# Kernel tuning notes

Hardware: AMD Instinct MI355X
Metric: run time of the kernel (lower is better)

Reference implementation:

```python
import jax, jax.numpy as jnp
import numpy as np

N_NODES = 50000
N_EDGES = 800000
N_GRAPHS = 512
IN_DIM, HID_DIM, EMB_DIM = 128, 256, 128
EPS = 1e-5


def setup_inputs() -> dict:
    key = jax.random.key(0)
    ks = jax.random.split(key, 12)
    x = jax.random.normal(ks[0], (N_NODES, IN_DIM), dtype=jnp.float32)
    edge_index = jax.random.randint(ks[1], (2, N_EDGES), 0, N_NODES, dtype=jnp.int32)
    batch = jnp.sort(jax.random.randint(ks[2], (N_NODES,), 0, N_GRAPHS, dtype=jnp.int32))
    s1 = 1.0 / np.sqrt(IN_DIM)
    s2 = 1.0 / np.sqrt(HID_DIM)
    return {
        "x": x,
        "edge_index": edge_index,
        "batch": batch,
        "W1": jax.random.uniform(ks[3], (IN_DIM, HID_DIM), jnp.float32, -s1, s1),
        "b1": jnp.zeros((HID_DIM,), jnp.float32),
        "gamma1": jnp.ones((HID_DIM,), jnp.float32),
        "beta1": jnp.zeros((HID_DIM,), jnp.float32),
        "W2": jax.random.uniform(ks[4], (HID_DIM, EMB_DIM), jnp.float32, -s2, s2),
        "b2": jnp.zeros((EMB_DIM,), jnp.float32),
        "gamma2": jnp.ones((EMB_DIM,), jnp.float32),
        "beta2": jnp.zeros((EMB_DIM,), jnp.float32),
    }


def _gcn_conv(x, W, b, src, dst, n_nodes):
    # PyG GCNConv: h = xW; aggregate with sym-normalized adjacency incl. self-loops; + bias
    h = x @ W  # [N, D]
    ones = jnp.ones(src.shape[0], dtype=h.dtype)
    deg = jax.ops.segment_sum(ones, dst, num_segments=n_nodes) + 1.0  # self-loop
    dinv = jax.lax.rsqrt(deg)
    norm = dinv[src] * dinv[dst]  # [E]
    msg = h[src] * norm[:, None]  # gather + scale  [E, D]
    agg = jax.ops.segment_sum(msg, dst, num_segments=n_nodes)
    agg = agg + h * (1.0 / deg)[:, None]  # self-loop contribution (norm = 1/deg)
    return agg + b


def _batchnorm(h, gamma, beta):
    mean = jnp.mean(h, axis=0)
    var = jnp.mean(jnp.square(h - mean), axis=0)  # biased, training mode
    return gamma * (h - mean) * jax.lax.rsqrt(var + EPS) + beta


def reference(x, edge_index, batch, W1, b1, gamma1, beta1, W2, b2, gamma2, beta2):
    src, dst = edge_index[0], edge_index[1]
    n = x.shape[0]
    h = _gcn_conv(x, W1, b1, src, dst, n)
    h = _batchnorm(jax.nn.relu(h), gamma1, beta1)
    h = _gcn_conv(h, W2, b2, src, dst, n)
    h = _batchnorm(jax.nn.relu(h), gamma2, beta2)
    return jax.ops.segment_max(h, batch, num_segments=N_GRAPHS)
```

## Files before the change

### kernel.cpp

```cpp
#include <hip/hip_runtime.h>
#include <math.h>

#define N_NODES 50000
#define N_EDGES 800000
#define N_GRAPHS 512
#define IN_DIM 128
#define HID_DIM 256
#define EMB_DIM 128
#define EPS 1e-5f
#define ELLW 64
#define NGROUP 8
#define GROUPN 6250
#define BLK_PER_GROUP 256
#define EPB ((N_EDGES + BLK_PER_GROUP - 1) / BLK_PER_GROUP)
#define F2B_N (N_NODES * IN_DIM / 4)
#define F2B_BLOCKS ((F2B_N + 255) / 256)
#define TW1_BLOCKS ((HID_DIM * IN_DIM + 255) / 256)

typedef __attribute__((ext_vector_type(8))) short bf16x8;
typedef __attribute__((ext_vector_type(4))) float f32x4;

static __device__ __forceinline__ unsigned short f2b(float f) {
    unsigned u = __float_as_uint(f);
    return (unsigned short)((u + 0x7fffu + ((u >> 16) & 1u)) >> 16);
}
static __device__ __forceinline__ float b2f(unsigned short h) {
    return __uint_as_float(((unsigned)h) << 16);
}

__global__ void __launch_bounds__(256) scatter_xcd(const int* __restrict__ src,
                                                   const int* __restrict__ dst,
                                                   int* __restrict__ fill,
                                                   int* __restrict__ col) {
    int b = blockIdx.x;
    int g = b & 7;
    int bs = b >> 3;
    int lo = g * GROUPN;
    int hi = lo + GROUPN;
    int e_end = min((bs + 1) * EPB, N_EDGES);
    for (int e = bs * EPB + threadIdx.x; e < e_end; e += 256) {
        int d = dst[e];
        if (d >= lo && d < hi) {
            int pos = atomicAdd(&fill[d], 1);
            pos = min(pos, ELLW - 1);
            col[(d << 6) + pos] = src[e];
        }
    }
}

__global__ void dinv_kernel(const int* __restrict__ fill, float* __restrict__ dinv) {
    int v = blockIdx.x * blockDim.x + threadIdx.x;
    if (v < N_NODES) dinv[v] = rsqrtf((float)(min(fill[v], ELLW) + 1));
}

__global__ void convert_kernel(const float* __restrict__ x, unsigned short* __restrict__ xbf,
                               const float* __restrict__ W1, unsigned short* __restrict__ W1t) {
    int b = blockIdx.x;
    if (b < F2B_BLOCKS) {
        int i = b * 256 + threadIdx.x;
        if (i < F2B_N) {
            float4 v = ((const float4*)x)[i];
            ushort4 o;
            o.x = f2b(v.x); o.y = f2b(v.y); o.z = f2b(v.z); o.w = f2b(v.w);
            ((ushort4*)xbf)[i] = o;
        }
    } else {
        int j = (b - F2B_BLOCKS) * 256 + threadIdx.x;
        if (j < HID_DIM * IN_DIM) {
            int n = j >> 7;
            int k = j & 127;
            W1t[j] = f2b(W1[k * HID_DIM + n]);
        }
    }
}

static __device__ __forceinline__ void acc8(float* acc, uint4 r, float w) {
    const unsigned* u = (const unsigned*)&r;
#pragma unroll
    for (int k = 0; k < 4; ++k) {
        float lo = __uint_as_float((u[k] & 0xFFFFu) << 16);
        float hi = __uint_as_float(u[k] & 0xFFFF0000u);
        acc[2 * k]     += w * lo;
        acc[2 * k + 1] += w * hi;
    }
}

template <bool RELU, bool OUT_BF, bool BIAS>
__global__ void __launch_bounds__(256) aggw_kernel(const unsigned short* __restrict__ h,
                                                   const float* __restrict__ dinv,
                                                   const int* __restrict__ deg,
                                                   const int* __restrict__ col,
                                                   const float* __restrict__ bias,
                                                   void* __restrict__ y) {
    int tid = threadIdx.x;
    int lane = tid & 63;
    int wid = tid >> 6;
    int v = blockIdx.x * 4 + wid;
    int g = lane >> 4;
    int p = lane & 15;

    int beg = v << 6;
    int end = beg + min(deg[v], ELLW);
    float acc[8] = {};

    for (int e = beg; e < end; e += 16) {
        int i0 = e + g, i1 = e + 4 + g, i2 = e + 8 + g, i3 = e + 12 + g;
        int c0 = min(i0, end - 1), c1 = min(i1, end - 1);
        int c2 = min(i2, end - 1), c3 = min(i3, end - 1);
        int u0 = col[c0], u1 = col[c1], u2 = col[c2], u3 = col[c3];
        float w0 = (i0 < end) ? dinv[u0] : 0.f;
        float w1 = (i1 < end) ? dinv[u1] : 0.f;
        float w2 = (i2 < end) ? dinv[u2] : 0.f;
        float w3 = (i3 < end) ? dinv[u3] : 0.f;
        uint4 d0 = *(const uint4*)(h + (size_t)u0 * 128 + p * 8);
        uint4 d1 = *(const uint4*)(h + (size_t)u1 * 128 + p * 8);
        uint4 d2 = *(const uint4*)(h + (size_t)u2 * 128 + p * 8);
        uint4 d3 = *(const uint4*)(h + (size_t)u3 * 128 + p * 8);
        acc8(acc, d0, w0);
        acc8(acc, d1, w1);
        acc8(acc, d2, w2);
        acc8(acc, d3, w3);
    }

#pragma unroll
    for (int k = 0; k < 8; ++k) {
        float a = acc[k];
        a += __shfl_xor(a, 16, 64);
        a += __shfl_xor(a, 32, 64);
        acc[k] = a;
    }

    if (g == 0) {
        uint4 selfr = *(const uint4*)(h + (size_t)v * 128 + p * 8);
        const unsigned* su = (const unsigned*)&selfr;
        float dv = dinv[v];
        float dv2 = dv * dv;
        float o[8];
#pragma unroll
        for (int k = 0; k < 4; ++k) {
            float lo = __uint_as_float((su[k] & 0xFFFFu) << 16);
            float hi = __uint_as_float(su[k] & 0xFFFF0000u);
            o[2 * k]     = dv * acc[2 * k]     + lo * dv2;
            o[2 * k + 1] = dv * acc[2 * k + 1] + hi * dv2;
        }
        if (BIAS) {
            float4 bv0 = *(const float4*)&bias[p * 8];
            float4 bv1 = *(const float4*)&bias[p * 8 + 4];
            o[0] += bv0.x; o[1] += bv0.y; o[2] += bv0.z; o[3] += bv0.w;
            o[4] += bv1.x; o[5] += bv1.y; o[6] += bv1.z; o[7] += bv1.w;
        }
        if (RELU) {
#pragma unroll
            for (int k = 0; k < 8; ++k) o[k] = fmaxf(o[k], 0.f);
        }
        if (OUT_BF) {
            uint4 packed;
            unsigned* pu = (unsigned*)&packed;
#pragma unroll
            for (int k = 0; k < 4; ++k)
                pu[k] = (unsigned)f2b(o[2 * k]) | ((unsigned)f2b(o[2 * k + 1]) << 16);
            *(uint4*)((unsigned short*)y + (size_t)v * 128 + p * 8) = packed;
        } else {
            float* yf = (float*)y + (size_t)v * 128 + p * 8;
            *(float4*)yf = make_float4(o[0], o[1], o[2], o[3]);
            *(float4*)(yf + 4) = make_float4(o[4], o[5], o[6], o[7]);
        }
    }
}

template <bool RELU>
__global__ void __launch_bounds__(256) mfma_gemm_kernel(const unsigned short* __restrict__ A,
                                                        const unsigned short* __restrict__ Bt,
                                                        const float* __restrict__ bias,
                                                        unsigned short* __restrict__ C,
                                                        int M, int N, int K) {
    const int LDT = 40;
    __shared__ unsigned short As[64 * LDT];
    __shared__ unsigned short Bs[64 * LDT];
    int tid = threadIdx.x;
    int bm = blockIdx.x * 64;
    int bn = blockIdx.y * 64;
    int lr = tid >> 2;
    int lc = (tid & 3) * 8;
    int lane = tid & 63;
    int w = tid >> 6;
    int wr = (w >> 1) * 32, wc = (w & 1) * 32;
    int l15 = lane & 15, q = lane >> 4;

    f32x4 acc[2][2] = {};
    bool arow_ok = (bm + lr) < M;
    const unsigned short* Aptr = A + (size_t)(bm + lr) * K + lc;
    const unsigned short* Bptr = Bt + (size_t)(bn + lr) * K + lc;

    for (int k0 = 0; k0 < K; k0 += 32) {
        uint4 av = arow_ok ? *(const uint4*)(Aptr + k0) : make_uint4(0u, 0u, 0u, 0u);
        uint4 bv = *(const uint4*)(Bptr + k0);
        *(uint4*)&As[lr * LDT + lc] = av;
        *(uint4*)&Bs[lr * LDT + lc] = bv;
        __syncthreads();
        bf16x8 a0 = *(const bf16x8*)&As[(wr + 0 + l15) * LDT + q * 8];
        bf16x8 a1 = *(const bf16x8*)&As[(wr + 16 + l15) * LDT + q * 8];
        bf16x8 b0 = *(const bf16x8*)&Bs[(wc + 0 + l15) * LDT + q * 8];
        bf16x8 b1 = *(const bf16x8*)&Bs[(wc + 16 + l15) * LDT + q * 8];
        acc[0][0] = __builtin_amdgcn_mfma_f32_16x16x32_bf16(a0, b0, acc[0][0], 0, 0, 0);
        acc[0][1] = __builtin_amdgcn_mfma_f32_16x16x32_bf16(a0, b1, acc[0][1], 0, 0, 0);
        acc[1][0] = __builtin_amdgcn_mfma_f32_16x16x32_bf16(a1, b0, acc[1][0], 0, 0, 0);
        acc[1][1] = __builtin_amdgcn_mfma_f32_16x16x32_bf16(a1, b1, acc[1][1], 0, 0, 0);
        __syncthreads();
    }

#pragma unroll
    for (int mi = 0; mi < 2; ++mi)
#pragma unroll
        for (int ni = 0; ni < 2; ++ni) {
            int colc = bn + wc + ni * 16 + l15;
            float bv = bias ? bias[colc] : 0.f;
#pragma unroll
            for (int r = 0; r < 4; ++r) {
                int row = bm + wr + mi * 16 + q * 4 + r;
                if (row < M) {
                    float vv = acc[mi][ni][r] + bv;
                    if (RELU) vv = fmaxf(vv, 0.f);
                    C[(size_t)row * N + colc] = f2b(vv);
                }
            }
        }
}

template <int C, bool BF>
__global__ void __launch_bounds__(256) stats_fast(const void* __restrict__ yv,
                                                  float* __restrict__ sum,
                                                  float* __restrict__ sumsq) {
    constexpr int VEC = BF ? 8 : 4;
    constexpr int NCHUNK = C / VEC;
    constexpr int ROWS = 256 / NCHUNK;
    constexpr int STRIDE = 256 * ROWS;
    __shared__ float sp[256 * VEC];
    __shared__ float qp[256 * VEC];
    int t = threadIdx.x;
    int j = t & (NCHUNK - 1);
    float s[VEC], q[VEC];
#pragma unroll
    for (int k = 0; k < VEC; ++k) { s[k] = 0.f; q[k] = 0.f; }

    const char* base = (const char*)yv + (size_t)j * 16;
    auto body = [&](int v) {
        uint4 raw = *(const uint4*)(base + (size_t)v * (C * (BF ? 2 : 4)));
        float x[VEC];
        if (BF) {
            const unsigned* u = (const unsigned*)&raw;
#pragma unroll
            for (int k = 0; k < 4; ++k) {
                x[2 * k]     = __uint_as_float((u[k] & 0xFFFFu) << 16);
                x[2 * k + 1] = __uint_as_float(u[k] & 0xFFFF0000u);
            }
        } else {
            const float* f = (const float*)&raw;
#pragma unroll
            for (int k = 0; k < VEC; ++k) x[k] = f[k];
        }
#pragma unroll
        for (int k = 0; k < VEC; ++k) { s[k] += x[k]; q[k] += x[k] * x[k]; }
    };

    int v = blockIdx.x * ROWS + (t >> 5);
    for (; v + 3 * STRIDE < N_NODES; v += 4 * STRIDE) {
        body(v); body(v + STRIDE); body(v + 2 * STRIDE); body(v + 3 * STRIDE);
    }
    for (; v < N_NODES; v += STRIDE) body(v);

#pragma unroll
    for (int k = 0; k < VEC; ++k) { sp[t * VEC + k] = s[k]; qp[t * VEC + k] = q[k]; }
    __syncthreads();
    if (t < C) {
        float ss = 0.f, qq = 0.f;
#pragma unroll
        for (int rr = 0; rr < ROWS; ++rr) {
            ss += sp[rr * (NCHUNK * VEC) + t];
            qq += qp[rr * (NCHUNK * VEC) + t];
        }
        atomicAdd(&sum[t], ss);
        atomicAdd(&sumsq[t], qq);
    }
}

__global__ void prep2_kernel(const float* __restrict__ sum1, const float* __restrict__ sumsq1,
                             const float* __restrict__ gamma1, const float* __restrict__ beta1,
                             const float* __restrict__ W2, unsigned short* __restrict__ W2pt,
                             float* __restrict__ bc2) {
    __shared__ float a1s[HID_DIM], s1s[HID_DIM];
    int t = threadIdx.x;
    {
        float m = sum1[t] * (1.f / N_NODES);
        float var = sumsq1[t] * (1.f / N_NODES) - m * m;
        float a = gamma1[t] * rsqrtf(var + EPS);
        a1s[t] = a;
        s1s[t] = beta1[t] - m * a;
    }
    __syncthreads();
    if (t < EMB_DIM) {
        float bacc = 0.f;
        for (int k = 0; k < HID_DIM; ++k) {
            float w = W2[k * EMB_DIM + t];
            W2pt[t * HID_DIM + k] = f2b(a1s[k] * w);
            bacc += s1s[k] * w;
        }
        bc2[t] = bacc;
    }
}

__global__ void prepa2_kernel(const float* __restrict__ sum2, const float* __restrict__ sumsq2,
                              const float* __restrict__ gamma2, const float* __restrict__ beta2,
                              float* __restrict__ a2, float* __restrict__ s2) {
    int t = threadIdx.x;
    float m = sum2[t] * (1.f / N_NODES);
    float var = sumsq2[t] * (1.f / N_NODES) - m * m;
    float a = gamma2[t] * rsqrtf(var + EPS);
    a2[t] = a;
    s2[t] = beta2[t] - m * a;
}

__global__ void __launch_bounds__(128) segmax_kernel(const float* __restrict__ y,
                                                     const float* __restrict__ a2,
                                                     const float* __restrict__ s2,
                                                     const int* __restrict__ batch,
                                                     float* __restrict__ out) {
    __shared__ int sh[2];
    int g = blockIdx.x;
    if (threadIdx.x == 0) {
        int lo = 0, hi = N_NODES;
        while (lo < hi) { int mid = (lo + hi) >> 1; if (batch[mid] < g) lo = mid + 1; else hi = mid; }
        sh[0] = lo;
        hi = N_NODES;
        while (lo < hi) { int mid = (lo + hi) >> 1; if (batch[mid] < g + 1) lo = mid + 1; else hi = mid; }
        sh[1] = lo;
    }
    __syncthreads();
    int beg = sh[0], end = sh[1];
    int c = threadIdx.x;
    float ac = a2[c], sc = s2[c];
    float m = -INFINITY;
    for (int v = beg; v < end; ++v) {
        m = fmaxf(m, fmaf(ac, y[(size_t)v * EMB_DIM + c], sc));
    }
    out[(size_t)g * EMB_DIM + c] = m;
}

extern "C" void kernel_launch(void* const* d_in, const int* in_sizes, int n_in,
                              void* d_out, int out_size, void* d_ws, size_t ws_size,
                              hipStream_t stream) {
    const float* x      = (const float*)d_in[0];
    const int*   ei     = (const int*)d_in[1];
    const int*   batch  = (const int*)d_in[2];
    const float* W1     = (const float*)d_in[3];
    const float* b1     = (const float*)d_in[4];
    const float* gamma1 = (const float*)d_in[5];
    const float* beta1  = (const float*)d_in[6];
    const float* W2     = (const float*)d_in[7];
    const float* b2     = (const float*)d_in[8];
    const float* gamma2 = (const float*)d_in[9];
    const float* beta2  = (const float*)d_in[10];
    float* out = (float*)d_out;

    char* ws = (char*)d_ws;
    size_t off = 0;
    auto alloc = [&](size_t bytes) -> char* {
        char* p = ws + off;
        off = (off + bytes + 255) & ~(size_t)255;
        return p;
    };
    int*   fill   = (int*)alloc((size_t)N_NODES * 4);
    int*   col    = (int*)alloc((size_t)N_NODES * ELLW * 4);
    float* dinv   = (float*)alloc((size_t)N_NODES * 4);
    float* stats  = (float*)alloc(1024 * 4);
    float* bc2    = (float*)alloc((size_t)EMB_DIM * 4);
    unsigned short* W1t  = (unsigned short*)alloc((size_t)HID_DIM * IN_DIM * 2);
    unsigned short* W2pt = (unsigned short*)alloc((size_t)HID_DIM * EMB_DIM * 2);
    unsigned short* xbf  = (unsigned short*)alloc((size_t)N_NODES * IN_DIM * 2);
    unsigned short* axbf = (unsigned short*)alloc((size_t)N_NODES * IN_DIM * 2);
    unsigned short* y1bf = (unsigned short*)alloc((size_t)N_NODES * HID_DIM * 2);
    unsigned short* gbf  = (unsigned short*)alloc((size_t)N_NODES * EMB_DIM * 2);
    float* y2 = (float*)xbf;
    (void)ws_size; (void)in_sizes; (void)n_in; (void)out_size;

    const int* src  = ei;
    const int* dstp = ei + N_EDGES;

    hipMemsetAsync(fill, 0, (size_t)N_NODES * 4, stream);
    hipMemsetAsync(stats, 0, 1024 * 4, stream);

    scatter_xcd<<<NGROUP * BLK_PER_GROUP, 256, 0, stream>>>(src, dstp, fill, col);
    dinv_kernel<<<(N_NODES + 255) / 256, 256, 0, stream>>>(fill, dinv);

    convert_kernel<<<F2B_BLOCKS + TW1_BLOCKS, 256, 0, stream>>>(x, xbf, W1, W1t);

    aggw_kernel<false, true, false><<<N_NODES / 4, 256, 0, stream>>>(xbf, dinv, fill, col, nullptr, axbf);
    dim3 g1((N_NODES + 63) / 64, HID_DIM / 64);
    mfma_gemm_kernel<true><<<g1, 256, 0, stream>>>(axbf, W1t, b1, y1bf, N_NODES, HID_DIM, IN_DIM);
    stats_fast<HID_DIM, true><<<256, 256, 0, stream>>>(y1bf, stats, stats + 256);

    prep2_kernel<<<1, 256, 0, stream>>>(stats, stats + 256, gamma1, beta1, W2, W2pt, bc2);

    dim3 g2((N_NODES + 63) / 64, EMB_DIM / 64);
    mfma_gemm_kernel<false><<<g2, 256, 0, stream>>>(y1bf, W2pt, bc2, gbf, N_NODES, EMB_DIM, HID_DIM);
    aggw_kernel<true, false, true><<<N_NODES / 4, 256, 0, stream>>>(gbf, dinv, fill, col, b2, y2);
    stats_fast<EMB_DIM, false><<<256, 256, 0, stream>>>(y2, stats + 512, stats + 640);

    prepa2_kernel<<<1, EMB_DIM, 0, stream>>>(stats + 512, stats + 640, gamma2, beta2,
                                             stats + 768, stats + 896);
    segmax_kernel<<<N_GRAPHS, 128, 0, stream>>>(y2, stats + 768, stats + 896, batch, out);
}
```

Measured before the change: 307.2 us.

## Fuse BN1 stats into GEMM epilogue, widen GEMM tile, merge small kernels

The first GEMM now computes per-column sum and sum-of-squares in its epilogue, reduced with shuffles and accumulated with atomics, so the separate stats pass over the hidden activations is gone. Both GEMMs switch to a 64x128 tile where each wave covers all 64 rows and 32 columns, which reuses A across more MFMAs. The dinv computation moves into the convert kernel, prepa2 folds into segmax, and the two memsets become one. The trade-offs are extra atomic traffic, fewer GEMM blocks with more registers per thread, and a different float summation order for the statistics.

```diff
diff --git a/kernel.cpp b/kernel.cpp
--- a/kernel.cpp
+++ b/kernel.cpp
@@ -16,6 +16,7 @@
 #define F2B_N (N_NODES * IN_DIM / 4)
 #define F2B_BLOCKS ((F2B_N + 255) / 256)
 #define TW1_BLOCKS ((HID_DIM * IN_DIM + 255) / 256)
+#define DINV_BLOCKS ((N_NODES + 255) / 256)
 
 typedef __attribute__((ext_vector_type(8))) short bf16x8;
 typedef __attribute__((ext_vector_type(4))) float f32x4;
@@ -48,13 +49,9 @@
     }
 }
 
-__global__ void dinv_kernel(const int* __restrict__ fill, float* __restrict__ dinv) {
-    int v = blockIdx.x * blockDim.x + threadIdx.x;
-    if (v < N_NODES) dinv[v] = rsqrtf((float)(min(fill[v], ELLW) + 1));
-}
-
 __global__ void convert_kernel(const float* __restrict__ x, unsigned short* __restrict__ xbf,
-                               const float* __restrict__ W1, unsigned short* __restrict__ W1t) {
+                               const float* __restrict__ W1, unsigned short* __restrict__ W1t,
+                               const int* __restrict__ fill, float* __restrict__ dinv) {
     int b = blockIdx.x;
     if (b < F2B_BLOCKS) {
         int i = b * 256 + threadIdx.x;
@@ -64,13 +61,16 @@
             o.x = f2b(v.x); o.y = f2b(v.y); o.z = f2b(v.z); o.w = f2b(v.w);
             ((ushort4*)xbf)[i] = o;
         }
-    } else {
+    } else if (b < F2B_BLOCKS + TW1_BLOCKS) {
         int j = (b - F2B_BLOCKS) * 256 + threadIdx.x;
         if (j < HID_DIM * IN_DIM) {
             int n = j >> 7;
             int k = j & 127;
             W1t[j] = f2b(W1[k * HID_DIM + n]);
         }
+    } else {
+        int v = (b - F2B_BLOCKS - TW1_BLOCKS) * 256 + threadIdx.x;
+        if (v < N_NODES) dinv[v] = rsqrtf((float)(min(fill[v], ELLW) + 1));
     }
 }
 
@@ -168,63 +168,92 @@
     }
 }
 
-template <bool RELU>
+template <bool RELU, bool STATS>
 __global__ void __launch_bounds__(256) mfma_gemm_kernel(const unsigned short* __restrict__ A,
                                                         const unsigned short* __restrict__ Bt,
                                                         const float* __restrict__ bias,
                                                         unsigned short* __restrict__ C,
+                                                        float* __restrict__ sum,
+                                                        float* __restrict__ sumsq,
                                                         int M, int N, int K) {
     const int LDT = 40;
     __shared__ unsigned short As[64 * LDT];
-    __shared__ unsigned short Bs[64 * LDT];
+    __shared__ unsigned short Bs[128 * LDT];
     int tid = threadIdx.x;
     int bm = blockIdx.x * 64;
-    int bn = blockIdx.y * 64;
+    int bn = blockIdx.y * 128;
     int lr = tid >> 2;
     int lc = (tid & 3) * 8;
     int lane = tid & 63;
     int w = tid >> 6;
-    int wr = (w >> 1) * 32, wc = (w & 1) * 32;
+    int wc = w * 32;
     int l15 = lane & 15, q = lane >> 4;
 
-    f32x4 acc[2][2] = {};
+    f32x4 acc[4][2] = {};
     bool arow_ok = (bm + lr) < M;
     const unsigned short* Aptr = A + (size_t)(bm + lr) * K + lc;
-    const unsigned short* Bptr = Bt + (size_t)(bn + lr) * K + lc;
+    const unsigned short* B0 = Bt + (size_t)(bn + lr) * K + lc;
+    const unsigned short* B1 = Bt + (size_t)(bn + lr + 64) * K + lc;
 
     for (int k0 = 0; k0 < K; k0 += 32) {
         uint4 av = arow_ok ? *(const uint4*)(Aptr + k0) : make_uint4(0u, 0u, 0u, 0u);
-        uint4 bv = *(const uint4*)(Bptr + k0);
+        uint4 b0v = *(const uint4*)(B0 + k0);
+        uint4 b1v = *(const uint4*)(B1 + k0);
         *(uint4*)&As[lr * LDT + lc] = av;
-        *(uint4*)&Bs[lr * LDT + lc] = bv;
+        *(uint4*)&Bs[lr * LDT + lc] = b0v;
+        *(uint4*)&Bs[(lr + 64) * LDT + lc] = b1v;
         __syncthreads();
-        bf16x8 a0 = *(const bf16x8*)&As[(wr + 0 + l15) * LDT + q * 8];
-        bf16x8 a1 = *(const bf16x8*)&As[(wr + 16 + l15) * LDT + q * 8];
-        bf16x8 b0 = *(const bf16x8*)&Bs[(wc + 0 + l15) * LDT + q * 8];
-        bf16x8 b1 = *(const bf16x8*)&Bs[(wc + 16 + l15) * LDT + q * 8];
-        acc[0][0] = __builtin_amdgcn_mfma_f32_16x16x32_bf16(a0, b0, acc[0][0], 0, 0, 0);
-        acc[0][1] = __builtin_amdgcn_mfma_f32_16x16x32_bf16(a0, b1, acc[0][1], 0, 0, 0);
-        acc[1][0] = __builtin_amdgcn_mfma_f32_16x16x32_bf16(a1, b0, acc[1][0], 0, 0, 0);
-        acc[1][1] = __builtin_amdgcn_mfma_f32_16x16x32_bf16(a1, b1, acc[1][1], 0, 0, 0);
+        bf16x8 af[4], bf[2];
+#pragma unroll
+        for (int mi = 0; mi < 4; ++mi)
+            af[mi] = *(const bf16x8*)&As[(mi * 16 + l15) * LDT + q * 8];
+#pragma unroll
+        for (int ni = 0; ni < 2; ++ni)
+            bf[ni] = *(const bf16x8*)&Bs[(wc + ni * 16 + l15) * LDT + q * 8];
+#pragma unroll
+        for (int mi = 0; mi < 4; ++mi)
+#pragma unroll
+            for (int ni = 0; ni < 2; ++ni)
+                acc[mi][ni] = __builtin_amdgcn_mfma_f32_16x16x32_bf16(af[mi], bf[ni], acc[mi][ni], 0, 0, 0);
         __syncthreads();
     }
 
-#pragma unroll
-    for (int mi = 0; mi < 2; ++mi)
-#pragma unroll
-        for (int ni = 0; ni < 2; ++ni) {
-            int colc = bn + wc + ni * 16 + l15;
-            float bv = bias ? bias[colc] : 0.f;
+    float s[2] = {0.f, 0.f}, sq[2] = {0.f, 0.f};
+#pragma unroll
+    for (int ni = 0; ni < 2; ++ni) {
+        int colc = bn + wc + ni * 16 + l15;
+        float bv = bias ? bias[colc] : 0.f;
+#pragma unroll
+        for (int mi = 0; mi < 4; ++mi) {
 #pragma unroll
             for (int r = 0; r < 4; ++r) {
-                int row = bm + wr + mi * 16 + q * 4 + r;
-                if (row < M) {
-                    float vv = acc[mi][ni][r] + bv;
-                    if (RELU) vv = fmaxf(vv, 0.f);
-                    C[(size_t)row * N + colc] = f2b(vv);
+                int row = bm + mi * 16 + q * 4 + r;
+                bool ok = row < M;
+                float vv = acc[mi][ni][r] + bv;
+                if (RELU) vv = fmaxf(vv, 0.f);
+                unsigned short us = f2b(vv);
+                if (ok) C[(size_t)row * N + colc] = us;
+                if (STATS) {
+                    float xr = ok ? b2f(us) : 0.f;
+                    s[ni] += xr;
+                    sq[ni] += xr * xr;
                 }
             }
         }
+    }
+    if (STATS) {
+#pragma unroll
+        for (int ni = 0; ni < 2; ++ni) {
+            float a = s[ni], b = sq[ni];
+            a += __shfl_xor(a, 16, 64); a += __shfl_xor(a, 32, 64);
+            b += __shfl_xor(b, 16, 64); b += __shfl_xor(b, 32, 64);
+            if (q == 0) {
+                int colc = bn + wc + ni * 16 + l15;
+                atomicAdd(&sum[colc], a);
+                atomicAdd(&sumsq[colc], b);
+            }
+        }
+    }
 }
 
 template <int C, bool BF>
@@ -309,24 +338,20 @@
     }
 }
 
-__global__ void prepa2_kernel(const float* __restrict__ sum2, const float* __restrict__ sumsq2,
-                              const float* __restrict__ gamma2, const float* __restrict__ beta2,
-                              float* __restrict__ a2, float* __restrict__ s2) {
-    int t = threadIdx.x;
-    float m = sum2[t] * (1.f / N_NODES);
-    float var = sumsq2[t] * (1.f / N_NODES) - m * m;
-    float a = gamma2[t] * rsqrtf(var + EPS);
-    a2[t] = a;
-    s2[t] = beta2[t] - m * a;
-}
-
 __global__ void __launch_bounds__(128) segmax_kernel(const float* __restrict__ y,
-                                                     const float* __restrict__ a2,
-                                                     const float* __restrict__ s2,
+                                                     const float* __restrict__ sum2,
+                                                     const float* __restrict__ sumsq2,
+                                                     const float* __restrict__ gamma2,
+                                                     const float* __restrict__ beta2,
                                                      const int* __restrict__ batch,
                                                      float* __restrict__ out) {
     __shared__ int sh[2];
     int g = blockIdx.x;
+    int c = threadIdx.x;
+    float mch = sum2[c] * (1.f / N_NODES);
+    float var = sumsq2[c] * (1.f / N_NODES) - mch * mch;
+    float ac = gamma2[c] * rsqrtf(var + EPS);
+    float sc = beta2[c] - mch * ac;
     if (threadIdx.x == 0) {
         int lo = 0, hi = N_NODES;
         while (lo < hi) { int mid = (lo + hi) >> 1; if (batch[mid] < g) lo = mid + 1; else hi = mid; }
@@ -337,8 +362,6 @@
     }
     __syncthreads();
     int beg = sh[0], end = sh[1];
-    int c = threadIdx.x;
-    float ac = a2[c], sc = s2[c];
     float m = -INFINITY;
     for (int v = beg; v < end; ++v) {
         m = fmaxf(m, fmaf(ac, y[(size_t)v * EMB_DIM + c], sc));
@@ -370,9 +393,10 @@
         return p;
     };
     int*   fill   = (int*)alloc((size_t)N_NODES * 4);
+    float* stats  = (float*)alloc(1024 * 4);
+    size_t zbytes = off;
     int*   col    = (int*)alloc((size_t)N_NODES * ELLW * 4);
     float* dinv   = (float*)alloc((size_t)N_NODES * 4);
-    float* stats  = (float*)alloc(1024 * 4);
     float* bc2    = (float*)alloc((size_t)EMB_DIM * 4);
     unsigned short* W1t  = (unsigned short*)alloc((size_t)HID_DIM * IN_DIM * 2);
     unsigned short* W2pt = (unsigned short*)alloc((size_t)HID_DIM * EMB_DIM * 2);
@@ -386,27 +410,27 @@
     const int* src  = ei;
     const int* dstp = ei + N_EDGES;
 
-    hipMemsetAsync(fill, 0, (size_t)N_NODES * 4, stream);
-    hipMemsetAsync(stats, 0, 1024 * 4, stream);
+    hipMemsetAsync(ws, 0, zbytes, stream);
 
     scatter_xcd<<<NGROUP * BLK_PER_GROUP, 256, 0, stream>>>(src, dstp, fill, col);
-    dinv_kernel<<<(N_NODES + 255) / 256, 256, 0, stream>>>(fill, dinv);
-
-    convert_kernel<<<F2B_BLOCKS + TW1_BLOCKS, 256, 0, stream>>>(x, xbf, W1, W1t);
+    convert_kernel<<<F2B_BLOCKS + TW1_BLOCKS + DINV_BLOCKS, 256, 0, stream>>>(
+        x, xbf, W1, W1t, fill, dinv);
 
     aggw_kernel<false, true, false><<<N_NODES / 4, 256, 0, stream>>>(xbf, dinv, fill, col, nullptr, axbf);
-    dim3 g1((N_NODES + 63) / 64, HID_DIM / 64);
-    mfma_gemm_kernel<true><<<g1, 256, 0, stream>>>(axbf, W1t, b1, y1bf, N_NODES, HID_DIM, IN_DIM);
-    stats_fast<HID_DIM, true><<<256, 256, 0, stream>>>(y1bf, stats, stats + 256);
+    dim3 g1((N_NODES + 63) / 64, HID_DIM / 128);
+    mfma_gemm_kernel<true, true><<<g1, 256, 0, stream>>>(axbf, W1t, b1, y1bf,
+                                                         stats, stats + 256,
+                                                         N_NODES, HID_DIM, IN_DIM);
 
     prep2_kernel<<<1, 256, 0, stream>>>(stats, stats + 256, gamma1, beta1, W2, W2pt, bc2);
 
-    dim3 g2((N_NODES + 63) / 64, EMB_DIM / 64);
-    mfma_gemm_kernel<false><<<g2, 256, 0, stream>>>(y1bf, W2pt, bc2, gbf, N_NODES, EMB_DIM, HID_DIM);
+    dim3 g2((N_NODES + 63) / 64, EMB_DIM / 128);
+    mfma_gemm_kernel<false, false><<<g2, 256, 0, stream>>>(y1bf, W2pt, bc2, gbf,
+                                                           nullptr, nullptr,
+                                                           N_NODES, EMB_DIM, HID_DIM);
     aggw_kernel<true, false, true><<<N_NODES / 4, 256, 0, stream>>>(gbf, dinv, fill, col, b2, y2);
     stats_fast<EMB_DIM, false><<<256, 256, 0, stream>>>(y2, stats + 512, stats + 640);
 
-    prepa2_kernel<<<1, EMB_DIM, 0, stream>>>(stats + 512, stats + 640, gamma2, beta2,
-                                             stats + 768, stats + 896);
-    segmax_kernel<<<N_GRAPHS, 128, 0, stream>>>(y2, stats + 768, stats + 896, batch, out);
-}
+    segmax_kernel<<<N_GRAPHS, 128, 0, stream>>>(y2, stats + 512, stats + 640,
+                                                gamma2, beta2, batch, out);
+}
```

Measured after the change: 319.0 us. +3.8%, slower.
